# Kernel optimization log

Hardware: AMD Instinct MI355X
Metric: run time of the kernel (lower is better)

## Reference

```python
import jax, jax.numpy as jnp
import numpy as np
from jax import lax

EPS = 1e-08


def setup_inputs() -> dict:
    key = jax.random.key(0)
    k1, k2, k3, k4 = jax.random.split(key, 4)
    b, cin, cout, hw, kk = 32, 256, 256, 64, 3
    fan_in = cin * kk * kk
    # kaiming_normal_(a=0, mode='fan_in', nonlinearity='leaky_relu') -> gain=sqrt(2), std=sqrt(2/fan_in)
    w_std = np.sqrt(2.0 / fan_in).astype(np.float32)
    return {
        "x": jax.random.normal(k1, (b, cin, hw, hw), dtype=jnp.float32),
        "y": jax.random.normal(k2, (b, cin), dtype=jnp.float32),
        "weight": jax.random.normal(k3, (cout, cin, kk, kk), dtype=jnp.float32) * w_std,
        "bias": jax.random.normal(k4, (cout,), dtype=jnp.float32) * 0.1,
    }


def _modulated_conv(x, y, weight, bias):
    # x: [b, cin, h, w]; y: [b, cin]; weight: [cout, cin, kh, kw]; bias: [cout]
    # modulate: per-sample scale of input channels
    w = weight[None] * (y[:, None, :, None, None] + 1.0)  # [b, cout, cin, kh, kw]
    # demodulate: normalize each (sample, out-channel) filter
    d = lax.rsqrt(jnp.sum(w * w, axis=(2, 3, 4), keepdims=True) + EPS)
    w = w * d

    def conv_one(xi, wi):
        # xi: [cin, h, w]; wi: [cout, cin, kh, kw]
        out = lax.conv_general_dilated(
            xi[None], wi, window_strides=(1, 1), padding="SAME",
            dimension_numbers=("NCHW", "OIHW", "NCHW"))
        return out[0]  # [cout, h, w]

    out = jax.vmap(conv_one)(x, w)  # [b, cout, h, w]
    return out + bias[None, :, None, None]


def reference(x, y, weight, bias):
    return _modulated_conv(x, y, weight, bias)
```

## Files before the change

kernel.cpp:

```cpp
#include <hip/hip_runtime.h>
#include <hip/hip_bf16.h>

typedef __attribute__((ext_vector_type(8))) short short8;
typedef __attribute__((ext_vector_type(4))) float f32x4;

#define XT_IMG_BYTES (66*66*256*2)
#define XT_TOTAL_BYTES (32LL*XT_IMG_BYTES)
#define WM_ROW_BYTES (2304*2)
#define WM_IMG_BYTES (256*WM_ROW_BYTES)

static __device__ __forceinline__ void async16(void* lds, const void* g) {
  __builtin_amdgcn_global_load_lds((const __attribute__((address_space(1))) void*)g,
                                   (__attribute__((address_space(3))) void*)lds, 16, 0, 0);
}
static __device__ __forceinline__ ushort f2bf(float f) {
  __hip_bfloat16 h = __float2bfloat16(f);
  return *reinterpret_cast<ushort*>(&h);
}

__global__ __launch_bounds__(256) void k_prep(const float* __restrict__ x,
                                              const float* __restrict__ W,
                                              const float* __restrict__ y,
                                              ushort* __restrict__ xT,
                                              ushort* __restrict__ wmod) {
  __shared__ float smem[64][68];
  const int bid = blockIdx.x;
  const int t   = threadIdx.x;

  if (bid < 8192) {
    const int b  = bid >> 8;
    const int h  = (bid >> 2) & 63;
    const int c0 = (bid & 3) << 6;
    const float* xp = x + (size_t)(b * 256 + c0) * 4096 + h * 64;
#pragma unroll
    for (int j = 0; j < 4; ++j) {
      const int lin = j * 1024 + t * 4;
      const int il = lin >> 6, c = lin & 63;
      *(float4*)&smem[il][c] = *(const float4*)(xp + (size_t)il * 4096 + c);
    }
    __syncthreads();
    const int q  = t & 7;
    const int w0 = t >> 3;
    ushort* op = xT + (size_t)b * (66 * 66 * 256) + ((size_t)(h + 1) * 66 + 1) * 256 + c0;
#pragma unroll
    for (int j = 0; j < 2; ++j) {
      const int wl = j * 32 + w0;
      short8 v;
#pragma unroll
      for (int k2 = 0; k2 < 8; ++k2) v[k2] = (short)f2bf(smem[8 * q + k2][wl]);
      *(short8*)(op + (size_t)wl * 256 + 8 * q) = v;
    }
  } else if (bid < 8448) {
    float* red = &smem[0][0];
    const int o = bid - 8192;
    const float* wp = W + (size_t)(o * 256 + t) * 9;
    float wr[9];
#pragma unroll
    for (int r = 0; r < 9; ++r) wr[r] = wp[r];
    float ss = 0.f;
#pragma unroll
    for (int r = 0; r < 9; ++r) ss += wr[r] * wr[r];
    const int lane = t & 63, wid = t >> 6;
#pragma unroll 1
    for (int b = 0; b < 32; ++b) {
      const float ym = y[b * 256 + t] + 1.0f;
      float v = ss * ym * ym;
#pragma unroll
      for (int k = 1; k < 64; k <<= 1) v += __shfl_xor(v, k, 64);
      if (lane == 0) red[wid] = v;
      __syncthreads();
      const float tot = red[0] + red[1] + red[2] + red[3];
      const float sc = rsqrtf(tot + 1e-8f) * ym;
      ushort* op = wmod + ((size_t)(b * 256 + o)) * 2304 + t;
#pragma unroll
      for (int r = 0; r < 9; ++r) op[r * 256] = f2bf(wr[r] * sc);
      __syncthreads();
    }
  } else {
    const int zb = bid - 8448;
    const int b  = zb >> 3;
    const int tt = ((zb & 7) << 8) | t;
    uint4* xT4 = (uint4*)xT;
    const uint4 z = make_uint4(0u, 0u, 0u, 0u);
    uint4* base = xT4 + (size_t)b * (66 * 66 * 32);
    uint4* r0  = base;
    uint4* r65 = base + (size_t)65 * 66 * 32;
    for (int i = tt; i < 2112; i += 2048) { r0[i] = z; r65[i] = z; }
    {
      int r = (tt >> 5) + 1, c = tt & 31;
      base[((size_t)r * 66 + 0)  * 32 + c] = z;
      base[((size_t)r * 66 + 65) * 32 + c] = z;
    }
  }
}

__global__ __launch_bounds__(512, 2) void k_gemm(const ushort* __restrict__ wmod,
                                                 const ushort* __restrict__ xT,
                                                 const float* __restrict__ bias,
                                                 float* __restrict__ out) {
  __shared__ ushort ldsA[2][16384];
  __shared__ ushort ldsB[2][16384];

  const int t  = threadIdx.x;
  const int bx = blockIdx.x;
  const int xcd = bx & 7;
  const int idx = bx >> 3;
  const int b   = xcd + ((idx >> 4) << 3);
  const int tn  = idx & 15;
  const int n0  = tn << 8;
  const int h0  = tn << 2;

  const int ln = t & 15;
  const int kq = (t >> 4) & 3;
  const int wv = t >> 6;
  const int wm = wv >> 2;
  const int wn = wv & 3;

  const char* wmodB = (const char*)wmod + (size_t)b * WM_IMG_BYTES;
  const char* xTB   = (const char*)xT   + (size_t)b * XT_IMG_BYTES;

  int gAoff[4], gBoff[4];
#pragma unroll
  for (int j = 0; j < 4; ++j) {
    const int s = j * 512 + t;
    const int row = s >> 3, g = s & 7;
    gAoff[j] = row * WM_ROW_BYTES + ((g ^ (row & 7)) << 4);
    const int hr = row >> 6, wc = row & 63;
    gBoff[j] = ((h0 + hr) * 66 + wc) * 512 + ((g ^ (row & 7)) << 4);
  }

  const int swz = ln & 7;
  const int g0 = ((0 | kq) ^ swz) << 3;
  const int g1 = ((4 | kq) ^ swz) << 3;
  const int aBase = (wm * 128 + ln) * 64;
  const int bBase = (wn * 64  + ln) * 64;

  f32x4 acc[8][4];
  const f32x4 z4 = {0.f, 0.f, 0.f, 0.f};
#pragma unroll
  for (int i = 0; i < 8; ++i)
#pragma unroll
    for (int j = 0; j < 4; ++j) acc[i][j] = z4;

#define LOAD_A(J, KO, BUF) async16(&ldsA[BUF][0] + ((J) * 512 + t) * 8, wmodB + gAoff[J] + (KO))
#define LOAD_B(J, KO, BUF) async16(&ldsB[BUF][0] + ((J) * 512 + t) * 8, xTB   + gBoff[J] + (KO))

#define MF(F, E, A, B) acc[F][E] = __builtin_amdgcn_mfma_f32_16x16x32_bf16(A, B, acc[F][E], 0, 0, 0)
#define FENCE() __builtin_amdgcn_sched_barrier(0)
#define BAR()   __builtin_amdgcn_s_barrier()
#define SGB(M, N) __builtin_amdgcn_sched_group_barrier((M), (N), 0)

  LOAD_A(0, 0, 0); LOAD_A(1, 0, 0); LOAD_A(2, 0, 0); LOAD_A(3, 0, 0);
  LOAD_B(0, 0, 0); LOAD_B(1, 0, 0); LOAD_B(2, 0, 0); LOAD_B(3, 0, 0);
  {
    const int koA1 = 128;
    const int koB1 = 128;
    LOAD_A(0, koA1, 1); LOAD_A(2, koA1, 1);
    LOAD_B(0, koB1, 1); LOAD_B(1, koB1, 1); LOAD_B(2, koB1, 1); LOAD_B(3, koB1, 1);
  }
  asm volatile("s_waitcnt vmcnt(6)" ::: "memory");
  FENCE(); BAR(); FENCE();

#pragma unroll 1
  for (int kt = 0; kt < 36; ++kt) {
    const int s = kt & 1, sn = s ^ 1;
    const ushort* bufA = &ldsA[s][0];
    const ushort* bufB = &ldsB[s][0];

    const int n1 = kt + 1;
    const int koA1 = (n1 >> 2) * 512 + ((n1 & 3) << 7);
    const int n2 = kt + 2;
    const int r2 = n2 >> 2;
    const int kh2 = r2 / 3, kw2 = r2 - kh2 * 3;
    const int koA2 = r2 * 512 + ((n2 & 3) << 7);
    const int koB2 = (kh2 * 66 + kw2) * 512 + ((n2 & 3) << 7);

    short8 A0 = *(const short8*)(bufA + aBase + 0 * 1024 + g0);
    short8 A1 = *(const short8*)(bufA + aBase + 1 * 1024 + g0);
    short8 A2 = *(const short8*)(bufA + aBase + 2 * 1024 + g0);
    short8 A3 = *(const short8*)(bufA + aBase + 3 * 1024 + g0);
    short8 B0 = *(const short8*)(bufB + bBase + 0 * 1024 + g0);
    short8 B1 = *(const short8*)(bufB + bBase + 1 * 1024 + g0);
    short8 B2 = *(const short8*)(bufB + bBase + 2 * 1024 + g0);
    short8 B3 = *(const short8*)(bufB + bBase + 3 * 1024 + g0);
    short8 A4 = *(const short8*)(bufA + aBase + 4 * 1024 + g0);
    short8 A5 = *(const short8*)(bufA + aBase + 5 * 1024 + g0);
    short8 A6 = *(const short8*)(bufA + aBase + 6 * 1024 + g0);
    short8 A7 = *(const short8*)(bufA + aBase + 7 * 1024 + g0);
    if (kt < 35) { LOAD_A(1, koA1, sn); LOAD_A(3, koA1, sn); }
    SGB(0x100, 12);
    __builtin_amdgcn_s_setprio(1);
    MF(0,0,A0,B0); MF(1,0,A1,B0); MF(2,0,A2,B0); MF(3,0,A3,B0);
    MF(0,1,A0,B1); MF(1,1,A1,B1); MF(2,1,A2,B1); MF(3,1,A3,B1);
    MF(0,2,A0,B2); MF(1,2,A1,B2); MF(2,2,A2,B2); MF(3,2,A3,B2);
    MF(0,3,A0,B3); MF(1,3,A1,B3); MF(2,3,A2,B3); MF(3,3,A3,B3);
    __builtin_amdgcn_s_setprio(0);
    SGB(0x8, 16);
    short8 C0 = *(const short8*)(bufA + aBase + 0 * 1024 + g1);
    short8 C1 = *(const short8*)(bufA + aBase + 1 * 1024 + g1);
    short8 C2 = *(const short8*)(bufA + aBase + 2 * 1024 + g1);
    short8 C3 = *(const short8*)(bufA + aBase + 3 * 1024 + g1);
    short8 D0 = *(const short8*)(bufB + bBase + 0 * 1024 + g1);
    short8 D1 = *(const short8*)(bufB + bBase + 1 * 1024 + g1);
    short8 D2 = *(const short8*)(bufB + bBase + 2 * 1024 + g1);
    short8 D3 = *(const short8*)(bufB + bBase + 3 * 1024 + g1);
    SGB(0x100, 8);
    __builtin_amdgcn_s_setprio(1);
    MF(4,0,A4,B0); MF(5,0,A5,B0); MF(6,0,A6,B0); MF(7,0,A7,B0);
    MF(4,1,A4,B1); MF(5,1,A5,B1); MF(6,1,A6,B1); MF(7,1,A7,B1);
    MF(4,2,A4,B2); MF(5,2,A5,B2); MF(6,2,A6,B2); MF(7,2,A7,B2);
    MF(4,3,A4,B3); MF(5,3,A5,B3); MF(6,3,A6,B3); MF(7,3,A7,B3);
    __builtin_amdgcn_s_setprio(0);
    SGB(0x8, 16);
    short8 C4 = *(const short8*)(bufA + aBase + 4 * 1024 + g1);
    short8 C5 = *(const short8*)(bufA + aBase + 5 * 1024 + g1);
    short8 C6 = *(const short8*)(bufA + aBase + 6 * 1024 + g1);
    short8 C7 = *(const short8*)(bufA + aBase + 7 * 1024 + g1);
    SGB(0x100, 4);
    __builtin_amdgcn_s_setprio(1);
    MF(0,0,C0,D0); MF(1,0,C1,D0); MF(2,0,C2,D0); MF(3,0,C3,D0);
    MF(0,1,C0,D1); MF(1,1,C1,D1); MF(2,1,C2,D1); MF(3,1,C3,D1);
    MF(0,2,C0,D2); MF(1,2,C1,D2); MF(2,2,C2,D2); MF(3,2,C3,D2);
    MF(0,3,C0,D3); MF(1,3,C1,D3); MF(2,3,C2,D3); MF(3,3,C3,D3);
    __builtin_amdgcn_s_setprio(0);
    SGB(0x8, 16);

    FENCE(); BAR(); FENCE();

    if (kt < 34) {
      LOAD_A(0, koA2, s); LOAD_A(2, koA2, s);
      LOAD_B(0, koB2, s); LOAD_B(1, koB2, s);
      LOAD_B(2, koB2, s); LOAD_B(3, koB2, s);
    }
    __builtin_amdgcn_s_setprio(1);
    MF(4,0,C4,D0); MF(5,0,C5,D0); MF(6,0,C6,D0); MF(7,0,C7,D0);
    MF(4,1,C4,D1); MF(5,1,C5,D1); MF(6,1,C6,D1); MF(7,1,C7,D1);
    MF(4,2,C4,D2); MF(5,2,C5,D2); MF(6,2,C6,D2); MF(7,2,C7,D2);
    MF(4,3,C4,D3); MF(5,3,C5,D3); MF(6,3,C6,D3); MF(7,3,C7,D3);
    __builtin_amdgcn_s_setprio(0);

    if (kt < 34) {
      asm volatile("s_waitcnt vmcnt(6)" ::: "memory");
    } else {
      asm volatile("s_waitcnt vmcnt(0)" ::: "memory");
    }
    FENCE(); BAR();
  }

  const float* bp = bias + wm * 128;
  float* outB = out + ((size_t)(b * 256 + wm * 128)) * 4096 + n0 + wn * 64 + ln;
#pragma unroll
  for (int mi = 0; mi < 8; ++mi) {
#pragma unroll
    for (int rg = 0; rg < 4; ++rg) {
      const int orow = mi * 16 + kq * 4 + rg;
      const float bv = bp[orow];
      float* po = outB + (size_t)orow * 4096;
#pragma unroll
      for (int ni = 0; ni < 4; ++ni) po[ni * 16] = acc[mi][ni][rg] + bv;
    }
  }
#undef LOAD_A
#undef LOAD_B
#undef MF
#undef FENCE
#undef BAR
#undef SGB
}

extern "C" void kernel_launch(void* const* d_in, const int* in_sizes, int n_in,
                              void* d_out, int out_size, void* d_ws, size_t ws_size,
                              hipStream_t stream) {
  const float* x    = (const float*)d_in[0];
  const float* y    = (const float*)d_in[1];
  const float* W    = (const float*)d_in[2];
  const float* bias = (const float*)d_in[3];
  float* out = (float*)d_out;

  ushort* xT   = (ushort*)d_ws;
  ushort* wmod = (ushort*)((char*)d_ws + (size_t)XT_TOTAL_BYTES);

  k_prep<<<8704, 256, 0, stream>>>(x, W, y, xT, wmod);
  k_gemm<<<512,  512, 0, stream>>>(wmod, xT, bias, out);
}
```

Before: 385.2 us.

## Restructure GEMM mainloop into 4-stage LDS ring with register double-buffered fragments

Replaces the 2-buffer, K=128-per-stage LDS pipeline with a 4-slot ring of K=64 stages, prefetching three stages ahead. MFMA fragments are double-buffered in registers so the LDS reads for the next stage overlap the current stage's 32 MFMAs, with one barrier per stage. The XOR swizzle is dropped in favour of a linear 64-byte-row layout. This trades deeper latency hiding for more barriers, more live registers, and possible LDS bank conflicts from the unswizzled layout.

```diff
diff --git a/kernel.cpp b/kernel.cpp
--- a/kernel.cpp
+++ b/kernel.cpp
@@ -98,8 +98,7 @@
                                                  const ushort* __restrict__ xT,
                                                  const float* __restrict__ bias,
                                                  float* __restrict__ out) {
-  __shared__ ushort ldsA[2][16384];
-  __shared__ ushort ldsB[2][16384];
+  __shared__ ushort lds[4 * 16384];
 
   const int t  = threadIdx.x;
   const int bx = blockIdx.x;
@@ -119,21 +118,16 @@
   const char* wmodB = (const char*)wmod + (size_t)b * WM_IMG_BYTES;
   const char* xTB   = (const char*)xT   + (size_t)b * XT_IMG_BYTES;
 
-  int gAoff[4], gBoff[4];
-#pragma unroll
-  for (int j = 0; j < 4; ++j) {
-    const int s = j * 512 + t;
-    const int row = s >> 3, g = s & 7;
-    gAoff[j] = row * WM_ROW_BYTES + ((g ^ (row & 7)) << 4);
-    const int hr = row >> 6, wc = row & 63;
-    gBoff[j] = ((h0 + hr) * 66 + wc) * 512 + ((g ^ (row & 7)) << 4);
-  }
-
-  const int swz = ln & 7;
-  const int g0 = ((0 | kq) ^ swz) << 3;
-  const int g1 = ((4 | kq) ^ swz) << 3;
-  const int aBase = (wm * 128 + ln) * 64;
-  const int bBase = (wn * 64  + ln) * 64;
+  const int rowA = t >> 2;
+  const int g16  = (t & 3) << 4;
+  const int gAoff0 = rowA * WM_ROW_BYTES + g16;
+  const int gAoff1 = (128 + rowA) * WM_ROW_BYTES + g16;
+  const int pix0 = rowA, pix1 = 128 + rowA;
+  const int gBoff0 = ((h0 + (pix0 >> 6)) * 66 + (pix0 & 63)) * 512 + g16;
+  const int gBoff1 = ((h0 + (pix1 >> 6)) * 66 + (pix1 & 63)) * 512 + g16;
+
+  const int aBase = (wm * 128 + ln) * 32 + kq * 8;
+  const int bBase = (wn * 64  + ln) * 32 + kq * 8;
 
   f32x4 acc[8][4];
   const f32x4 z4 = {0.f, 0.f, 0.f, 0.f};
@@ -142,110 +136,106 @@
 #pragma unroll
     for (int j = 0; j < 4; ++j) acc[i][j] = z4;
 
-#define LOAD_A(J, KO, BUF) async16(&ldsA[BUF][0] + ((J) * 512 + t) * 8, wmodB + gAoff[J] + (KO))
-#define LOAD_B(J, KO, BUF) async16(&ldsB[BUF][0] + ((J) * 512 + t) * 8, xTB   + gBoff[J] + (KO))
-
-#define MF(F, E, A, B) acc[F][E] = __builtin_amdgcn_mfma_f32_16x16x32_bf16(A, B, acc[F][E], 0, 0, 0)
+  short8 FA0, FA1, FA2, FA3, FA4, FA5, FA6, FA7, FB0, FB1, FB2, FB3;
+  short8 NA0, NA1, NA2, NA3, NA4, NA5, NA6, NA7, NB0, NB1, NB2, NB3;
+
+#define MFC(MI, NI, A, B) acc[MI][NI] = __builtin_amdgcn_mfma_f32_16x16x32_bf16(A, B, acc[MI][NI], 0, 0, 0)
 #define FENCE() __builtin_amdgcn_sched_barrier(0)
 #define BAR()   __builtin_amdgcn_s_barrier()
 #define SGB(M, N) __builtin_amdgcn_sched_group_barrier((M), (N), 0)
 
-  LOAD_A(0, 0, 0); LOAD_A(1, 0, 0); LOAD_A(2, 0, 0); LOAD_A(3, 0, 0);
-  LOAD_B(0, 0, 0); LOAD_B(1, 0, 0); LOAD_B(2, 0, 0); LOAD_B(3, 0, 0);
+#define MFMA32(C)                                                                             \
+    MFC(0,0,C##A0,C##B0); MFC(1,0,C##A1,C##B0); MFC(2,0,C##A2,C##B0); MFC(3,0,C##A3,C##B0);   \
+    MFC(4,0,C##A4,C##B0); MFC(5,0,C##A5,C##B0); MFC(6,0,C##A6,C##B0); MFC(7,0,C##A7,C##B0);   \
+    MFC(0,1,C##A0,C##B1); MFC(1,1,C##A1,C##B1); MFC(2,1,C##A2,C##B1); MFC(3,1,C##A3,C##B1);   \
+    MFC(4,1,C##A4,C##B1); MFC(5,1,C##A5,C##B1); MFC(6,1,C##A6,C##B1); MFC(7,1,C##A7,C##B1);   \
+    MFC(0,2,C##A0,C##B2); MFC(1,2,C##A1,C##B2); MFC(2,2,C##A2,C##B2); MFC(3,2,C##A3,C##B2);   \
+    MFC(4,2,C##A4,C##B2); MFC(5,2,C##A5,C##B2); MFC(6,2,C##A6,C##B2); MFC(7,2,C##A7,C##B2);   \
+    MFC(0,3,C##A0,C##B3); MFC(1,3,C##A1,C##B3); MFC(2,3,C##A2,C##B3); MFC(3,3,C##A3,C##B3);   \
+    MFC(4,3,C##A4,C##B3); MFC(5,3,C##A5,C##B3); MFC(6,3,C##A6,C##B3); MFC(7,3,C##A7,C##B3)
+
+#define BODY(J, C, R, SEN, VMN) do {                                          \
+    const int j_ = (J);                                                       \
+    asm volatile("s_waitcnt lgkmcnt(0)" ::: "memory");                        \
+    FENCE();                                                                  \
+    const ushort* sA_ = lds + (((j_ + 1) & 3) << 14);                         \
+    const ushort* sB_ = sA_ + 8192;                                           \
+    R##A0 = *(const short8*)(sA_ + aBase + 0 * 512);                          \
+    R##A1 = *(const short8*)(sA_ + aBase + 1 * 512);                          \
+    R##A2 = *(const short8*)(sA_ + aBase + 2 * 512);                          \
+    R##A3 = *(const short8*)(sA_ + aBase + 3 * 512);                          \
+    R##A4 = *(const short8*)(sA_ + aBase + 4 * 512);                          \
+    R##A5 = *(const short8*)(sA_ + aBase + 5 * 512);                          \
+    R##A6 = *(const short8*)(sA_ + aBase + 6 * 512);                          \
+    R##A7 = *(const short8*)(sA_ + aBase + 7 * 512);                          \
+    R##B0 = *(const short8*)(sB_ + bBase + 0 * 512);                          \
+    R##B1 = *(const short8*)(sB_ + bBase + 1 * 512);                          \
+    R##B2 = *(const short8*)(sB_ + bBase + 2 * 512);                          \
+    R##B3 = *(const short8*)(sB_ + bBase + 3 * 512);                          \
+    if (SEN) {                                                                \
+      const int n3_ = j_ + 3;                                                 \
+      const int r3_ = n3_ >> 3;                                               \
+      const int kh3_ = r3_ / 3, kw3_ = r3_ - kh3_ * 3;                        \
+      const int koA3_ = r3_ * 512 + ((n3_ & 7) << 6);                         \
+      const int koB3_ = (kh3_ * 66 + kw3_) * 512 + ((n3_ & 7) << 6);          \
+      char* dst_ = (char*)lds + ((n3_ & 3) << 15);                            \
+      async16(dst_ + t * 16,          wmodB + gAoff0 + koA3_);                \
+      async16(dst_ + 8192 + t * 16,   wmodB + gAoff1 + koA3_);                \
+      async16(dst_ + 16384 + t * 16,  xTB + gBoff0 + koB3_);                  \
+      async16(dst_ + 24576 + t * 16,  xTB + gBoff1 + koB3_);                  \
+    }                                                                         \
+    __builtin_amdgcn_s_setprio(1);                                            \
+    MFMA32(C);                                                                \
+    __builtin_amdgcn_s_setprio(0);                                            \
+    SGB(0x100, 4); SGB(0x8, 8);                                               \
+    SGB(0x100, 4); SGB(0x8, 8);                                               \
+    if (SEN) { SGB(0x30, 4); }                                                \
+    SGB(0x100, 4); SGB(0x8, 8);                                               \
+    SGB(0x8, 8);                                                              \
+    asm volatile("s_waitcnt vmcnt(" VMN ")" ::: "memory");                    \
+    FENCE(); BAR(); FENCE();                                                  \
+  } while (0)
+
+#pragma unroll
+  for (int kt = 0; kt < 3; ++kt) {
+    char* dst = (char*)lds + (kt << 15);
+    const int ko = kt << 6;
+    async16(dst + t * 16,         wmodB + gAoff0 + ko);
+    async16(dst + 8192 + t * 16,  wmodB + gAoff1 + ko);
+    async16(dst + 16384 + t * 16, xTB + gBoff0 + ko);
+    async16(dst + 24576 + t * 16, xTB + gBoff1 + ko);
+  }
+  asm volatile("s_waitcnt vmcnt(4)" ::: "memory");
+  FENCE(); BAR(); FENCE();
+
   {
-    const int koA1 = 128;
-    const int koB1 = 128;
-    LOAD_A(0, koA1, 1); LOAD_A(2, koA1, 1);
-    LOAD_B(0, koB1, 1); LOAD_B(1, koB1, 1); LOAD_B(2, koB1, 1); LOAD_B(3, koB1, 1);
-  }
-  asm volatile("s_waitcnt vmcnt(6)" ::: "memory");
-  FENCE(); BAR(); FENCE();
+    const ushort* sA_ = lds;
+    const ushort* sB_ = lds + 8192;
+    FA0 = *(const short8*)(sA_ + aBase + 0 * 512);
+    FA1 = *(const short8*)(sA_ + aBase + 1 * 512);
+    FA2 = *(const short8*)(sA_ + aBase + 2 * 512);
+    FA3 = *(const short8*)(sA_ + aBase + 3 * 512);
+    FA4 = *(const short8*)(sA_ + aBase + 4 * 512);
+    FA5 = *(const short8*)(sA_ + aBase + 5 * 512);
+    FA6 = *(const short8*)(sA_ + aBase + 6 * 512);
+    FA7 = *(const short8*)(sA_ + aBase + 7 * 512);
+    FB0 = *(const short8*)(sB_ + bBase + 0 * 512);
+    FB1 = *(const short8*)(sB_ + bBase + 1 * 512);
+    FB2 = *(const short8*)(sB_ + bBase + 2 * 512);
+    FB3 = *(const short8*)(sB_ + bBase + 3 * 512);
+  }
 
 #pragma unroll 1
-  for (int kt = 0; kt < 36; ++kt) {
-    const int s = kt & 1, sn = s ^ 1;
-    const ushort* bufA = &ldsA[s][0];
-    const ushort* bufB = &ldsB[s][0];
-
-    const int n1 = kt + 1;
-    const int koA1 = (n1 >> 2) * 512 + ((n1 & 3) << 7);
-    const int n2 = kt + 2;
-    const int r2 = n2 >> 2;
-    const int kh2 = r2 / 3, kw2 = r2 - kh2 * 3;
-    const int koA2 = r2 * 512 + ((n2 & 3) << 7);
-    const int koB2 = (kh2 * 66 + kw2) * 512 + ((n2 & 3) << 7);
-
-    short8 A0 = *(const short8*)(bufA + aBase + 0 * 1024 + g0);
-    short8 A1 = *(const short8*)(bufA + aBase + 1 * 1024 + g0);
-    short8 A2 = *(const short8*)(bufA + aBase + 2 * 1024 + g0);
-    short8 A3 = *(const short8*)(bufA + aBase + 3 * 1024 + g0);
-    short8 B0 = *(const short8*)(bufB + bBase + 0 * 1024 + g0);
-    short8 B1 = *(const short8*)(bufB + bBase + 1 * 1024 + g0);
-    short8 B2 = *(const short8*)(bufB + bBase + 2 * 1024 + g0);
-    short8 B3 = *(const short8*)(bufB + bBase + 3 * 1024 + g0);
-    short8 A4 = *(const short8*)(bufA + aBase + 4 * 1024 + g0);
-    short8 A5 = *(const short8*)(bufA + aBase + 5 * 1024 + g0);
-    short8 A6 = *(const short8*)(bufA + aBase + 6 * 1024 + g0);
-    short8 A7 = *(const short8*)(bufA + aBase + 7 * 1024 + g0);
-    if (kt < 35) { LOAD_A(1, koA1, sn); LOAD_A(3, koA1, sn); }
-    SGB(0x100, 12);
-    __builtin_amdgcn_s_setprio(1);
-    MF(0,0,A0,B0); MF(1,0,A1,B0); MF(2,0,A2,B0); MF(3,0,A3,B0);
-    MF(0,1,A0,B1); MF(1,1,A1,B1); MF(2,1,A2,B1); MF(3,1,A3,B1);
-    MF(0,2,A0,B2); MF(1,2,A1,B2); MF(2,2,A2,B2); MF(3,2,A3,B2);
-    MF(0,3,A0,B3); MF(1,3,A1,B3); MF(2,3,A2,B3); MF(3,3,A3,B3);
-    __builtin_amdgcn_s_setprio(0);
-    SGB(0x8, 16);
-    short8 C0 = *(const short8*)(bufA + aBase + 0 * 1024 + g1);
-    short8 C1 = *(const short8*)(bufA + aBase + 1 * 1024 + g1);
-    short8 C2 = *(const short8*)(bufA + aBase + 2 * 1024 + g1);
-    short8 C3 = *(const short8*)(bufA + aBase + 3 * 1024 + g1);
-    short8 D0 = *(const short8*)(bufB + bBase + 0 * 1024 + g1);
-    short8 D1 = *(const short8*)(bufB + bBase + 1 * 1024 + g1);
-    short8 D2 = *(const short8*)(bufB + bBase + 2 * 1024 + g1);
-    short8 D3 = *(const short8*)(bufB + bBase + 3 * 1024 + g1);
-    SGB(0x100, 8);
-    __builtin_amdgcn_s_setprio(1);
-    MF(4,0,A4,B0); MF(5,0,A5,B0); MF(6,0,A6,B0); MF(7,0,A7,B0);
-    MF(4,1,A4,B1); MF(5,1,A5,B1); MF(6,1,A6,B1); MF(7,1,A7,B1);
-    MF(4,2,A4,B2); MF(5,2,A5,B2); MF(6,2,A6,B2); MF(7,2,A7,B2);
-    MF(4,3,A4,B3); MF(5,3,A5,B3); MF(6,3,A6,B3); MF(7,3,A7,B3);
-    __builtin_amdgcn_s_setprio(0);
-    SGB(0x8, 16);
-    short8 C4 = *(const short8*)(bufA + aBase + 4 * 1024 + g1);
-    short8 C5 = *(const short8*)(bufA + aBase + 5 * 1024 + g1);
-    short8 C6 = *(const short8*)(bufA + aBase + 6 * 1024 + g1);
-    short8 C7 = *(const short8*)(bufA + aBase + 7 * 1024 + g1);
-    SGB(0x100, 4);
-    __builtin_amdgcn_s_setprio(1);
-    MF(0,0,C0,D0); MF(1,0,C1,D0); MF(2,0,C2,D0); MF(3,0,C3,D0);
-    MF(0,1,C0,D1); MF(1,1,C1,D1); MF(2,1,C2,D1); MF(3,1,C3,D1);
-    MF(0,2,C0,D2); MF(1,2,C1,D2); MF(2,2,C2,D2); MF(3,2,C3,D2);
-    MF(0,3,C0,D3); MF(1,3,C1,D3); MF(2,3,C2,D3); MF(3,3,C3,D3);
-    __builtin_amdgcn_s_setprio(0);
-    SGB(0x8, 16);
-
-    FENCE(); BAR(); FENCE();
-
-    if (kt < 34) {
-      LOAD_A(0, koA2, s); LOAD_A(2, koA2, s);
-      LOAD_B(0, koB2, s); LOAD_B(1, koB2, s);
-      LOAD_B(2, koB2, s); LOAD_B(3, koB2, s);
-    }
-    __builtin_amdgcn_s_setprio(1);
-    MF(4,0,C4,D0); MF(5,0,C5,D0); MF(6,0,C6,D0); MF(7,0,C7,D0);
-    MF(4,1,C4,D1); MF(5,1,C5,D1); MF(6,1,C6,D1); MF(7,1,C7,D1);
-    MF(4,2,C4,D2); MF(5,2,C5,D2); MF(6,2,C6,D2); MF(7,2,C7,D2);
-    MF(4,3,C4,D3); MF(5,3,C5,D3); MF(6,3,C6,D3); MF(7,3,C7,D3);
-    __builtin_amdgcn_s_setprio(0);
-
-    if (kt < 34) {
-      asm volatile("s_waitcnt vmcnt(6)" ::: "memory");
-    } else {
-      asm volatile("s_waitcnt vmcnt(0)" ::: "memory");
-    }
-    FENCE(); BAR();
-  }
+  for (int j = 0; j < 68; j += 2) {
+    BODY(j,     F, N, 1, "4");
+    BODY(j + 1, N, F, 1, "4");
+  }
+  BODY(68, F, N, 1, "4");
+  BODY(69, N, F, 0, "0");
+  BODY(70, F, N, 0, "0");
+  asm volatile("s_waitcnt lgkmcnt(0)" ::: "memory");
+  FENCE();
+  MFMA32(N);
 
   const float* bp = bias + wm * 128;
   float* outB = out + ((size_t)(b * 256 + wm * 128)) * 4096 + n0 + wn * 64 + ln;
@@ -260,12 +250,12 @@
       for (int ni = 0; ni < 4; ++ni) po[ni * 16] = acc[mi][ni][rg] + bv;
     }
   }
-#undef LOAD_A
-#undef LOAD_B
-#undef MF
+#undef MFC
 #undef FENCE
 #undef BAR
 #undef SGB
+#undef MFMA32
+#undef BODY
 }
 
 extern "C" void kernel_launch(void* const* d_in, const int* in_sizes, int n_in,
```

After: 386.4 us. Within noise of the previous version (+0.3%).
